# Kernel optimization log

Measured on AMD Instinct MI355X. Metric: run time of the kernel, lower is better.

## Reference

```python
import jax, jax.numpy as jnp
import numpy as np

B, R, L, K = 64, 196, 512, 768
NEG = jnp.float32(-2**31 + 1)


def setup_inputs() -> dict:
    key = jax.random.key(0)
    ks = jax.random.split(key, 8)
    image_emb = jax.random.normal(ks[0], (B, R, L), dtype=jnp.float32)
    seq_emb = jax.random.normal(ks[1], (B, L, K), dtype=jnp.float32)
    mask = jax.random.randint(ks[2], (B, L), 0, 2, dtype=jnp.int32)
    # Linear(l,1) and Linear(k,1) params, Xavier-ish scale
    image_W = jax.random.normal(ks[3], (L, 1), dtype=jnp.float32) / np.sqrt(L)
    image_b = jnp.zeros((1,), dtype=jnp.float32)
    seq_W = jax.random.normal(ks[4], (K, 1), dtype=jnp.float32) / np.sqrt(K)
    seq_b = jnp.zeros((1,), dtype=jnp.float32)
    # V_weight [L, L], xavier_uniform
    lim = np.sqrt(6.0 / (L + L)).astype(np.float32)
    V_weight = jax.random.uniform(ks[5], (L, L), dtype=jnp.float32, minval=-lim, maxval=lim)
    return {"image_emb": image_emb, "seq_emb": seq_emb, "mask": mask,
            "image_W": image_W, "image_b": image_b,
            "seq_W": seq_W, "seq_b": seq_b, "V_weight": V_weight}


def reference(image_emb, seq_emb, mask, image_W, image_b, seq_W, seq_b, V_weight):
    # p: [B,R,1], q: [B,L,1]
    p = jnp.tanh(image_emb @ image_W + image_b)
    q = jnp.tanh(seq_emb @ seq_W + seq_b)
    qt = jnp.swapaxes(q, 1, 2)              # [B,1,L]
    emb = p @ qt + qt                       # [B,R,L] (rank-1 outer + broadcast add)
    score = emb @ V_weight                  # [B,R,L]
    # dropout_rate=0.0 -> identity
    score = jnp.where(mask[:, None, :] == 0, NEG, score)
    score = jax.nn.softmax(score, axis=-1)  # [B,R,L]
    out = score @ seq_emb                   # [B,R,K]
    out = out / jnp.sqrt(jnp.float32(seq_emb.shape[-1]))
    return out
```

## Files before the change

### kernel.cpp

```cpp
#include <hip/hip_runtime.h>
#include <cstdint>
#include <cstddef>


typedef __attribute__((ext_vector_type(8))) short short8;
typedef __attribute__((ext_vector_type(4))) float f32x4;

__device__ __forceinline__ unsigned short f32_to_bf16(float x) {
    unsigned int u = __float_as_uint(x);
    unsigned int r = (u + 0x7FFFu + ((u >> 16) & 1u)) >> 16;
    return (unsigned short)r;
}
__device__ __forceinline__ float bf16_to_f32(unsigned short h) {
    return __uint_as_float(((unsigned int)h) << 16);
}

#if defined(__has_builtin)
#if __has_builtin(__builtin_amdgcn_cvt_pk_bf16_f32)
#define HAVE_PK_BF16 1
#endif
#endif

__device__ __forceinline__ unsigned int pk_bf16(float a, float b) {
#ifdef HAVE_PK_BF16
    typedef __attribute__((ext_vector_type(2))) __bf16 bf16x2;
    bf16x2 v = __builtin_amdgcn_cvt_pk_bf16_f32(a, b);
    return __builtin_bit_cast(unsigned int, v);
#else
    return (unsigned int)f32_to_bf16(a) | ((unsigned int)f32_to_bf16(b) << 16);
#endif
}

__global__ __launch_bounds__(256) void kprep(const float* __restrict__ seq,
                                             const float* __restrict__ seqW,
                                             const float* __restrict__ seqBias,
                                             const float* __restrict__ img,
                                             const float* __restrict__ imgW,
                                             const float* __restrict__ imgBias,
                                             unsigned short* __restrict__ seqT,
                                             float* __restrict__ qv,
                                             float* __restrict__ pv) {
    __shared__ __align__(16) unsigned int sT[128 * 32];
    __shared__ __align__(16) float sW[768];

    if (blockIdx.x >= 512) {
        int wv = threadIdx.x >> 6, lane = threadIdx.x & 63;
        int row = (blockIdx.x - 512) * 4 + wv;
        const float4* x4 = (const float4*)(img + (size_t)row * 512);
        const float4* w4 = (const float4*)imgW;
        float s = 0.f;
#pragma unroll
        for (int i = 0; i < 2; ++i) {
            float4 a = x4[i * 64 + lane];
            float4 c = w4[i * 64 + lane];
            s += a.x * c.x + a.y * c.y + a.z * c.z + a.w * c.w;
        }
#pragma unroll
        for (int o = 32; o; o >>= 1) s += __shfl_xor(s, o, 64);
        if (lane == 0) pv[row] = tanhf(s + imgBias[0]);
        return;
    }

    int b = blockIdx.x >> 3, jt = blockIdx.x & 7;
    int j0 = jt * 64;
    int t = threadIdx.x;
    sW[t] = seqW[t]; sW[t + 256] = seqW[t + 256]; sW[t + 512] = seqW[t + 512];

    int quad = t >> 4, kseg = t & 15;
    int qk = quad ^ kseg;
    const float* base = seq + (size_t)b * 512 * 768 + (size_t)(j0 + quad * 4) * 768;
    int jg = t & 7, krow = t >> 3;
    unsigned short* dst0 = seqT + (size_t)b * 768 * 512 + j0;
    float qp[4] = {0.f, 0.f, 0.f, 0.f};
    __syncthreads();

    for (int ck = 0; ck < 6; ++ck) {
        if (ck) __syncthreads();
#pragma unroll
        for (int rp = 0; rp < 2; ++rp) {
            int kq = rp * 64 + kseg * 4;
            int kg = ck * 128 + kq;
            float4 r0 = *(const float4*)(base + 0 * 768 + kg);
            float4 r1 = *(const float4*)(base + 1 * 768 + kg);
            float4 r2 = *(const float4*)(base + 2 * 768 + kg);
            float4 r3 = *(const float4*)(base + 3 * 768 + kg);
            float4 w  = *(const float4*)(sW + kg);
            qp[0] += r0.x * w.x + r0.y * w.y + r0.z * w.z + r0.w * w.w;
            qp[1] += r1.x * w.x + r1.y * w.y + r1.z * w.z + r1.w * w.w;
            qp[2] += r2.x * w.x + r2.y * w.y + r2.z * w.z + r2.w * w.w;
            qp[3] += r3.x * w.x + r3.y * w.y + r3.z * w.z + r3.w * w.w;
            float a0[4] = {r0.x, r0.y, r0.z, r0.w};
            float a1[4] = {r1.x, r1.y, r1.z, r1.w};
            float a2[4] = {r2.x, r2.y, r2.z, r2.w};
            float a3[4] = {r3.x, r3.y, r3.z, r3.w};
#pragma unroll
            for (int i = 0; i < 4; ++i) {
                int k = kq + i;
                int col = (qk ^ (i << 2)) & 15;
                uint2 v;
                v.x = pk_bf16(a0[i], a1[i]);
                v.y = pk_bf16(a2[i], a3[i]);
                *(uint2*)(sT + k * 32 + col * 2) = v;
            }
        }
        __syncthreads();
        unsigned short* dst = dst0 + (size_t)ck * 128 * 512;
#pragma unroll
        for (int wp = 0; wp < 4; ++wp) {
            int k = wp * 32 + krow;
            int s = ((k >> 2) & 15) ^ ((k & 3) << 2);
            int c0 = ((jg << 1) ^ s) & 15;
            int c1 = ((jg << 1) ^ 1 ^ s) & 15;
            uint2 va = *(const uint2*)(sT + k * 32 + c0 * 2);
            uint2 vb = *(const uint2*)(sT + k * 32 + c1 * 2);
            uint4 o;
            o.x = va.x; o.y = va.y; o.z = vb.x; o.w = vb.y;
            *(uint4*)(dst + (size_t)k * 512 + jg * 8) = o;
        }
    }
#pragma unroll
    for (int rr = 0; rr < 4; ++rr) {
        float s = qp[rr];
        s += __shfl_xor(s, 8, 64);
        s += __shfl_xor(s, 4, 64);
        s += __shfl_xor(s, 2, 64);
        s += __shfl_xor(s, 1, 64);
        if (kseg == 0) qv[b * 512 + j0 + quad * 4 + rr] = tanhf(s + seqBias[0]);
    }
}

__global__ __launch_bounds__(256) void krows_p(const float* __restrict__ x,
                                               const float* __restrict__ w,
                                               const float* __restrict__ bias,
                                               float* __restrict__ outp) {
    int wv = threadIdx.x >> 6, lane = threadIdx.x & 63;
    int row = blockIdx.x * 4 + wv;
    const float4* x4 = (const float4*)(x + (size_t)row * 512);
    const float4* w4 = (const float4*)w;
    float s = 0.f;
#pragma unroll
    for (int i = 0; i < 2; ++i) {
        float4 a = x4[i * 64 + lane];
        float4 c = w4[i * 64 + lane];
        s += a.x * c.x + a.y * c.y + a.z * c.z + a.w * c.w;
    }
#pragma unroll
    for (int o = 32; o; o >>= 1) s += __shfl_xor(s, o, 64);
    if (lane == 0) outp[row] = tanhf(s + bias[0]);
}

__global__ __launch_bounds__(256) void krows_q(const float* __restrict__ x,
                                               const float* __restrict__ w,
                                               const float* __restrict__ bias,
                                               float* __restrict__ outp) {
    int wv = threadIdx.x >> 6, lane = threadIdx.x & 63;
    int row = blockIdx.x * 4 + wv;
    const float4* x4 = (const float4*)(x + (size_t)row * 768);
    const float4* w4 = (const float4*)w;
    float s = 0.f;
#pragma unroll
    for (int i = 0; i < 3; ++i) {
        float4 a = x4[i * 64 + lane];
        float4 c = w4[i * 64 + lane];
        s += a.x * c.x + a.y * c.y + a.z * c.z + a.w * c.w;
    }
#pragma unroll
    for (int o = 32; o; o >>= 1) s += __shfl_xor(s, o, 64);
    if (lane == 0) outp[row] = tanhf(s + bias[0]);
}

__global__ __launch_bounds__(256) void kw(const float* __restrict__ qv,
                                          const float* __restrict__ V,
                                          const int* __restrict__ mask,
                                          float* __restrict__ wm) {
    __shared__ __align__(16) float sq[512];
    __shared__ __align__(16) float sacc[8][32][4];
    int b = blockIdx.x >> 2, jc = blockIdx.x & 3;
    int t = threadIdx.x;
    sq[t] = qv[b * 512 + t];
    sq[t + 256] = qv[b * 512 + t + 256];
    __syncthreads();
    int jt = t & 31, lg = t >> 5;
    const float4* V4 = (const float4*)V;
    int col4 = jc * 32 + jt;
    float ax = 0.f, ay = 0.f, az = 0.f, aw = 0.f;
    int lbase = lg * 64;
#pragma unroll 8
    for (int li = 0; li < 64; ++li) {
        int l = lbase + li;
        float qq = sq[l];
        float4 v = V4[(size_t)l * 128 + col4];
        ax += qq * v.x; ay += qq * v.y; az += qq * v.z; aw += qq * v.w;
    }
    sacc[lg][jt][0] = ax; sacc[lg][jt][1] = ay;
    sacc[lg][jt][2] = az; sacc[lg][jt][3] = aw;
    __syncthreads();
    if (t < 32) {
        float sx = 0.f, sy = 0.f, sz = 0.f, sw = 0.f;
#pragma unroll
        for (int g = 0; g < 8; ++g) {
            sx += sacc[g][t][0]; sy += sacc[g][t][1];
            sz += sacc[g][t][2]; sw += sacc[g][t][3];
        }
        const int* mrow = mask + b * 512 + jc * 128 + t * 4;
        float4 o;
        o.x = mrow[0] ? sx : -1e30f;
        o.y = mrow[1] ? sy : -1e30f;
        o.z = mrow[2] ? sz : -1e30f;
        o.w = mrow[3] ? sw : -1e30f;
        ((float4*)(wm + b * 512 + jc * 128))[t] = o;
    }
}

__global__ __launch_bounds__(256, 2) void kattn2(const unsigned short* __restrict__ seqT,
                                                 const float* __restrict__ p,
                                                 const float* __restrict__ wm,
                                                 float* __restrict__ out) {
    __shared__ __align__(16) unsigned short sB[2][128 * 64];
    __shared__ __align__(16) float swm[512];
    __shared__ float sinvz[64];
    __shared__ float sred[16];

    int raw = blockIdx.x;
    int g  = ((raw >> 5) << 3) + (raw & 7);
    int rt = (raw >> 3) & 3;
    int b  = g / 6, nt = g - b * 6;
    int t  = threadIdx.x;
    int wv = t >> 6, lane = t & 63;
    int mm = lane & 15, q = lane >> 4;
    int nb = nt * 128;

    float v0 = wm[b * 512 + t];
    float v1 = wm[b * 512 + t + 256];
    swm[t] = v0; swm[t + 256] = v1;
    float lmax = fmaxf(v0, v1);
    float fa = (v0 > -1e29f) ? v0 : 1e30f;
    float fb = (v1 > -1e29f) ? v1 : 1e30f;
    float lmin = fminf(fa, fb);
#pragma unroll
    for (int o = 32; o; o >>= 1) {
        lmax = fmaxf(lmax, __shfl_xor(lmax, o, 64));
        lmin = fminf(lmin, __shfl_xor(lmin, o, 64));
    }
    if (lane == 0) { sred[wv] = lmax; sred[8 + wv] = lmin; }
    __syncthreads();
    float wmax = fmaxf(fmaxf(sred[0], sred[1]), fmaxf(sred[2], sred[3]));
    float wmin = fminf(fminf(sred[8], sred[9]), fminf(sred[10], sred[11]));

    int rl = wv * 16 + mm;
    int r  = rt * 64 + rl;
    bool valid = r < 196;
    int pidx = b * 196 + (valid ? r : 195);
    float c = 1.0f + p[pidx];
    float M = (c >= 0.f) ? c * wmax : c * wmin;

    short8 afrag[16];
    float zsum = 0.f;
    const f32x4* swm4 = (const f32x4*)swm;
#pragma unroll
    for (int tk = 0; tk < 16; ++tk) {
        int jb = tk * 32 + q * 8;
        f32x4 w0 = swm4[jb >> 2];
        f32x4 w1 = swm4[(jb >> 2) + 1];
        short8 af;
#pragma unroll
        for (int jj = 0; jj < 8; ++jj) {
            float ww = (jj < 4) ? w0[jj] : w1[jj - 4];
            float e = valid ? __expf(c * ww - M) : 0.f;
            unsigned short h = f32_to_bf16(e);
            zsum += bf16_to_f32(h);
            af[jj] = (short)h;
        }
        afrag[tk] = af;
    }
    zsum += __shfl_xor(zsum, 16, 64);
    zsum += __shfl_xor(zsum, 32, 64);
    if (q == 0) sinvz[rl] = 1.0f / zsum;

    f32x4 acc[8];
#pragma unroll
    for (int s = 0; s < 8; ++s) acc[s] = (f32x4){0.f, 0.f, 0.f, 0.f};

    const unsigned short* seqTb = seqT + (size_t)b * 768 * 512 + (size_t)nb * 512;
    int nrow = t >> 3, jg = t & 7;
    auto stage = [&](int ch, int buf) {
        unsigned short* sb = sB[buf];
#pragma unroll
        for (int pp = 0; pp < 4; ++pp) {
            int n = pp * 32 + nrow;
            short8 v = *(const short8*)(seqTb + (size_t)n * 512 + ch * 64 + jg * 8);
            int sw = (n ^ (n >> 3)) & 7;
            *(short8*)(sb + n * 64 + ((jg ^ sw) << 3)) = v;
        }
    };

    __syncthreads();
    stage(0, 0);
    __syncthreads();
#pragma unroll
    for (int ch = 0; ch < 8; ++ch) {
        if (ch < 7) stage(ch + 1, (ch + 1) & 1);
        const unsigned short* cb = sB[ch & 1];
#pragma unroll
        for (int kk = 0; kk < 2; ++kk) {
            short8 bfr[8];
#pragma unroll
            for (int s = 0; s < 8; ++s) {
                int n = s * 16 + mm;
                int sw = (n ^ (n >> 3)) & 7;
                bfr[s] = *(const short8*)(cb + n * 64 + ((((kk << 2) + q) ^ sw) << 3));
            }
#pragma unroll
            for (int s = 0; s < 8; ++s)
                acc[s] = __builtin_amdgcn_mfma_f32_16x16x32_bf16(
                    afrag[(ch << 1) + kk], bfr[s], acc[s], 0, 0, 0);
        }
        __syncthreads();
    }

    const float invsqrtk = 0.036084391824351615f;
#pragma unroll
    for (int reg = 0; reg < 4; ++reg) {
        int row = q * 4 + reg;
        int rr = rt * 64 + wv * 16 + row;
        if (rr < 196) {
            float scale = sinvz[wv * 16 + row] * invsqrtk;
            float* op = out + (size_t)(b * 196 + rr) * 768 + nb + mm;
#pragma unroll
            for (int s = 0; s < 8; ++s)
                op[s * 16] = acc[s][reg] * scale;
        }
    }
}

__global__ __launch_bounds__(256, 2) void kattn(const float* __restrict__ seq,
                                                const float* __restrict__ p,
                                                const float* __restrict__ wm,
                                                float* __restrict__ out) {
    __shared__ __align__(16) unsigned int sseq[2][128 * 32];
    __shared__ __align__(16) float swm[512];
    __shared__ float sinvz[64];
    __shared__ float sred[16];

    int id = blockIdx.x;
    int rt = id & 3;
    int nt = (id >> 2) % 6;
    int b  = id / 24;
    int t  = threadIdx.x;
    int wv = t >> 6, lane = t & 63;
    int mm = lane & 15, q = lane >> 4;
    int nb = nt * 128;

    float v0 = wm[b * 512 + t];
    float v1 = wm[b * 512 + t + 256];
    swm[t] = v0; swm[t + 256] = v1;
    float lmax = fmaxf(v0, v1);
    float fa = (v0 > -1e29f) ? v0 : 1e30f;
    float fb = (v1 > -1e29f) ? v1 : 1e30f;
    float lmin = fminf(fa, fb);
#pragma unroll
    for (int o = 32; o; o >>= 1) {
        lmax = fmaxf(lmax, __shfl_xor(lmax, o, 64));
        lmin = fminf(lmin, __shfl_xor(lmin, o, 64));
    }
    if (lane == 0) { sred[wv] = lmax; sred[8 + wv] = lmin; }
    __syncthreads();
    float wmax = fmaxf(fmaxf(sred[0], sred[1]), fmaxf(sred[2], sred[3]));
    float wmin = fminf(fminf(sred[8], sred[9]), fminf(sred[10], sred[11]));

    int rl = wv * 16 + mm;
    int r  = rt * 64 + rl;
    bool valid = r < 196;
    int pidx = b * 196 + (valid ? r : 195);
    float c = 1.0f + p[pidx];
    float M = (c >= 0.f) ? c * wmax : c * wmin;

    short8 afrag[16];
    float zsum = 0.f;
    const f32x4* swm4 = (const f32x4*)swm;
#pragma unroll
    for (int tk = 0; tk < 16; ++tk) {
        int jb = tk * 32 + q * 8;
        f32x4 w0 = swm4[jb >> 2];
        f32x4 w1 = swm4[(jb >> 2) + 1];
        short8 af;
#pragma unroll
        for (int jj = 0; jj < 8; ++jj) {
            float ww = (jj < 4) ? w0[jj] : w1[jj - 4];
            float e = valid ? __expf(c * ww - M) : 0.f;
            unsigned short h = f32_to_bf16(e);
            zsum += bf16_to_f32(h);
            af[jj] = (short)h;
        }
        afrag[tk] = af;
    }
    zsum += __shfl_xor(zsum, 16, 64);
    zsum += __shfl_xor(zsum, 32, 64);
    if (q == 0) sinvz[rl] = 1.0f / zsum;

    f32x4 acc[8];
#pragma unroll
    for (int s = 0; s < 8; ++s) acc[s] = (f32x4){0.f, 0.f, 0.f, 0.f};

    const float* seqb = seq + (size_t)b * 512 * 768 + nb;
    int tl = t & 31, jp = t >> 5;
    int n0 = tl * 4;
    auto stage = [&](int ch, int buf) {
        unsigned int* sb = sseq[buf];
#pragma unroll
        for (int pass = 0; pass < 4; ++pass) {
            int jl = pass * 16 + jp * 2;
            int jglob = ch * 64 + jl;
            float4 a0 = *(const float4*)(seqb + (size_t)jglob * 768 + n0);
            float4 a1 = *(const float4*)(seqb + (size_t)(jglob + 1) * 768 + n0);
            float a0v[4] = {a0.x, a0.y, a0.z, a0.w};
            float a1v[4] = {a1.x, a1.y, a1.z, a1.w};
            int g = jl >> 3;
            int wo = (jl & 7) >> 1;
#pragma unroll
            for (int i = 0; i < 4; ++i) {
                int n = n0 + i;
                int sw = (n ^ (n >> 3)) & 7;
                unsigned int pk = (unsigned int)f32_to_bf16(a0v[i]) |
                                  ((unsigned int)f32_to_bf16(a1v[i]) << 16);
                sb[n * 32 + ((g ^ sw) << 2) + wo] = pk;
            }
        }
    };

    __syncthreads();
    stage(0, 0);
    __syncthreads();
#pragma unroll
    for (int ch = 0; ch < 8; ++ch) {
        if (ch < 7) stage(ch + 1, (ch + 1) & 1);
        const unsigned int* cb = sseq[ch & 1];
#pragma unroll
        for (int kk = 0; kk < 2; ++kk) {
            short8 bfr[8];
#pragma unroll
            for (int s = 0; s < 8; ++s) {
                int n = s * 16 + mm;
                int g = kk * 4 + q;
                int sw = (n ^ (n >> 3)) & 7;
                bfr[s] = *(const short8*)(cb + n * 32 + ((g ^ sw) << 2));
            }
#pragma unroll
            for (int s = 0; s < 8; ++s)
                acc[s] = __builtin_amdgcn_mfma_f32_16x16x32_bf16(
                    afrag[ch * 2 + kk], bfr[s], acc[s], 0, 0, 0);
        }
        __syncthreads();
    }

    const float invsqrtk = 0.036084391824351615f;
#pragma unroll
    for (int reg = 0; reg < 4; ++reg) {
        int row = q * 4 + reg;
        int rr = rt * 64 + wv * 16 + row;
        if (rr < 196) {
            float scale = sinvz[wv * 16 + row] * invsqrtk;
            float* op = out + (size_t)(b * 196 + rr) * 768 + nb + mm;
#pragma unroll
            for (int s = 0; s < 8; ++s)
                op[s * 16] = acc[s][reg] * scale;
        }
    }
}

extern "C" void kernel_launch(void* const* d_in, const int* in_sizes, int n_in,
                              void* d_out, int out_size, void* d_ws, size_t ws_size,
                              hipStream_t stream) {
    const float* image_emb = (const float*)d_in[0];
    const float* seq_emb   = (const float*)d_in[1];
    const int*   mask      = (const int*)d_in[2];
    const float* image_W   = (const float*)d_in[3];
    const float* image_b   = (const float*)d_in[4];
    const float* seq_W     = (const float*)d_in[5];
    const float* seq_b     = (const float*)d_in[6];
    const float* V         = (const float*)d_in[7];
    float* out = (float*)d_out;

    float* p_ws  = (float*)d_ws;
    float* q_ws  = (float*)((char*)d_ws + (64 << 10));
    float* wm_ws = (float*)((char*)d_ws + (192 << 10));
    unsigned short* seqT = (unsigned short*)((char*)d_ws + (384 << 10));

    size_t need = (size_t)(384 << 10) + (size_t)64 * 768 * 512 * 2;
    if (ws_size >= need) {
        kprep<<<dim3(3648), dim3(256), 0, stream>>>(seq_emb, seq_W, seq_b,
                                                    image_emb, image_W, image_b,
                                                    seqT, q_ws, p_ws);
        kw<<<dim3(256), dim3(256), 0, stream>>>(q_ws, V, mask, wm_ws);
        kattn2<<<dim3(1536), dim3(256), 0, stream>>>(seqT, p_ws, wm_ws, out);
    } else {
        krows_p<<<dim3(3136), dim3(256), 0, stream>>>(image_emb, image_W, image_b, p_ws);
        krows_q<<<dim3(8192), dim3(256), 0, stream>>>(seq_emb, seq_W, seq_b, q_ws);
        kw<<<dim3(256), dim3(256), 0, stream>>>(q_ws, V, mask, wm_ws);
        kattn<<<dim3(1536), dim3(256), 0, stream>>>(seq_emb, p_ws, wm_ws, out);
    }
}
```

Measured before the change: 239.1 us.

## Split seq transpose/projection across K chunks with atomic partial sums

```diff
diff --git a/kernel.cpp b/kernel.cpp
--- a/kernel.cpp
+++ b/kernel.cpp
@@ -33,19 +33,18 @@
 
 __global__ __launch_bounds__(256) void kprep(const float* __restrict__ seq,
                                              const float* __restrict__ seqW,
-                                             const float* __restrict__ seqBias,
                                              const float* __restrict__ img,
                                              const float* __restrict__ imgW,
                                              const float* __restrict__ imgBias,
                                              unsigned short* __restrict__ seqT,
-                                             float* __restrict__ qv,
+                                             float* __restrict__ qacc,
                                              float* __restrict__ pv) {
     __shared__ __align__(16) unsigned int sT[128 * 32];
-    __shared__ __align__(16) float sW[768];
-
-    if (blockIdx.x >= 512) {
+    __shared__ __align__(16) float sWc[128];
+
+    if (blockIdx.x >= 3072) {
         int wv = threadIdx.x >> 6, lane = threadIdx.x & 63;
-        int row = (blockIdx.x - 512) * 4 + wv;
+        int row = (blockIdx.x - 3072) * 4 + wv;
         const float4* x4 = (const float4*)(img + (size_t)row * 512);
         const float4* w4 = (const float4*)imgW;
         float s = 0.f;
@@ -61,62 +60,59 @@
         return;
     }
 
-    int b = blockIdx.x >> 3, jt = blockIdx.x & 7;
+    int id = blockIdx.x;
+    int b = id / 48, rem = id - b * 48;
+    int jt = rem / 6, ck = rem - jt * 6;
     int j0 = jt * 64;
     int t = threadIdx.x;
-    sW[t] = seqW[t]; sW[t + 256] = seqW[t + 256]; sW[t + 512] = seqW[t + 512];
+    if (t < 128) sWc[t] = seqW[ck * 128 + t];
 
     int quad = t >> 4, kseg = t & 15;
     int qk = quad ^ kseg;
-    const float* base = seq + (size_t)b * 512 * 768 + (size_t)(j0 + quad * 4) * 768;
+    const float* base = seq + (size_t)b * 512 * 768 + (size_t)(j0 + quad * 4) * 768 + ck * 128;
     int jg = t & 7, krow = t >> 3;
-    unsigned short* dst0 = seqT + (size_t)b * 768 * 512 + j0;
     float qp[4] = {0.f, 0.f, 0.f, 0.f};
     __syncthreads();
 
-    for (int ck = 0; ck < 6; ++ck) {
-        if (ck) __syncthreads();
-#pragma unroll
-        for (int rp = 0; rp < 2; ++rp) {
-            int kq = rp * 64 + kseg * 4;
-            int kg = ck * 128 + kq;
-            float4 r0 = *(const float4*)(base + 0 * 768 + kg);
-            float4 r1 = *(const float4*)(base + 1 * 768 + kg);
-            float4 r2 = *(const float4*)(base + 2 * 768 + kg);
-            float4 r3 = *(const float4*)(base + 3 * 768 + kg);
-            float4 w  = *(const float4*)(sW + kg);
-            qp[0] += r0.x * w.x + r0.y * w.y + r0.z * w.z + r0.w * w.w;
-            qp[1] += r1.x * w.x + r1.y * w.y + r1.z * w.z + r1.w * w.w;
-            qp[2] += r2.x * w.x + r2.y * w.y + r2.z * w.z + r2.w * w.w;
-            qp[3] += r3.x * w.x + r3.y * w.y + r3.z * w.z + r3.w * w.w;
-            float a0[4] = {r0.x, r0.y, r0.z, r0.w};
-            float a1[4] = {r1.x, r1.y, r1.z, r1.w};
-            float a2[4] = {r2.x, r2.y, r2.z, r2.w};
-            float a3[4] = {r3.x, r3.y, r3.z, r3.w};
-#pragma unroll
-            for (int i = 0; i < 4; ++i) {
-                int k = kq + i;
-                int col = (qk ^ (i << 2)) & 15;
-                uint2 v;
-                v.x = pk_bf16(a0[i], a1[i]);
-                v.y = pk_bf16(a2[i], a3[i]);
-                *(uint2*)(sT + k * 32 + col * 2) = v;
-            }
-        }
-        __syncthreads();
-        unsigned short* dst = dst0 + (size_t)ck * 128 * 512;
-#pragma unroll
-        for (int wp = 0; wp < 4; ++wp) {
-            int k = wp * 32 + krow;
-            int s = ((k >> 2) & 15) ^ ((k & 3) << 2);
-            int c0 = ((jg << 1) ^ s) & 15;
-            int c1 = ((jg << 1) ^ 1 ^ s) & 15;
-            uint2 va = *(const uint2*)(sT + k * 32 + c0 * 2);
-            uint2 vb = *(const uint2*)(sT + k * 32 + c1 * 2);
-            uint4 o;
-            o.x = va.x; o.y = va.y; o.z = vb.x; o.w = vb.y;
-            *(uint4*)(dst + (size_t)k * 512 + jg * 8) = o;
-        }
+#pragma unroll
+    for (int rp = 0; rp < 2; ++rp) {
+        int kq = rp * 64 + kseg * 4;
+        float4 r0 = *(const float4*)(base + 0 * 768 + kq);
+        float4 r1 = *(const float4*)(base + 1 * 768 + kq);
+        float4 r2 = *(const float4*)(base + 2 * 768 + kq);
+        float4 r3 = *(const float4*)(base + 3 * 768 + kq);
+        float4 w  = *(const float4*)(sWc + kq);
+        qp[0] += r0.x * w.x + r0.y * w.y + r0.z * w.z + r0.w * w.w;
+        qp[1] += r1.x * w.x + r1.y * w.y + r1.z * w.z + r1.w * w.w;
+        qp[2] += r2.x * w.x + r2.y * w.y + r2.z * w.z + r2.w * w.w;
+        qp[3] += r3.x * w.x + r3.y * w.y + r3.z * w.z + r3.w * w.w;
+        float a0[4] = {r0.x, r0.y, r0.z, r0.w};
+        float a1[4] = {r1.x, r1.y, r1.z, r1.w};
+        float a2[4] = {r2.x, r2.y, r2.z, r2.w};
+        float a3[4] = {r3.x, r3.y, r3.z, r3.w};
+#pragma unroll
+        for (int i = 0; i < 4; ++i) {
+            int k = kq + i;
+            int col = (qk ^ (i << 2)) & 15;
+            uint2 v;
+            v.x = pk_bf16(a0[i], a1[i]);
+            v.y = pk_bf16(a2[i], a3[i]);
+            *(uint2*)(sT + k * 32 + col * 2) = v;
+        }
+    }
+    __syncthreads();
+    unsigned short* dst = seqT + (size_t)b * 768 * 512 + (size_t)ck * 128 * 512 + j0;
+#pragma unroll
+    for (int wp = 0; wp < 4; ++wp) {
+        int k = wp * 32 + krow;
+        int s = ((k >> 2) & 15) ^ ((k & 3) << 2);
+        int c0 = ((jg << 1) ^ s) & 15;
+        int c1 = ((jg << 1) ^ 1 ^ s) & 15;
+        uint2 va = *(const uint2*)(sT + k * 32 + c0 * 2);
+        uint2 vb = *(const uint2*)(sT + k * 32 + c1 * 2);
+        uint4 o;
+        o.x = va.x; o.y = va.y; o.z = vb.x; o.w = vb.y;
+        *(uint4*)(dst + (size_t)k * 512 + jg * 8) = o;
     }
 #pragma unroll
     for (int rr = 0; rr < 4; ++rr) {
@@ -125,7 +121,7 @@
         s += __shfl_xor(s, 4, 64);
         s += __shfl_xor(s, 2, 64);
         s += __shfl_xor(s, 1, 64);
-        if (kseg == 0) qv[b * 512 + j0 + quad * 4 + rr] = tanhf(s + seqBias[0]);
+        if (kseg == 0) atomicAdd(qacc + b * 512 + j0 + quad * 4 + rr, s);
     }
 }
 
@@ -151,7 +147,6 @@
 
 __global__ __launch_bounds__(256) void krows_q(const float* __restrict__ x,
                                                const float* __restrict__ w,
-                                               const float* __restrict__ bias,
                                                float* __restrict__ outp) {
     int wv = threadIdx.x >> 6, lane = threadIdx.x & 63;
     int row = blockIdx.x * 4 + wv;
@@ -166,10 +161,11 @@
     }
 #pragma unroll
     for (int o = 32; o; o >>= 1) s += __shfl_xor(s, o, 64);
-    if (lane == 0) outp[row] = tanhf(s + bias[0]);
-}
-
-__global__ __launch_bounds__(256) void kw(const float* __restrict__ qv,
+    if (lane == 0) outp[row] = s;
+}
+
+__global__ __launch_bounds__(256) void kw(const float* __restrict__ qacc,
+                                          const float* __restrict__ seqBias,
                                           const float* __restrict__ V,
                                           const int* __restrict__ mask,
                                           float* __restrict__ wm) {
@@ -177,8 +173,9 @@
     __shared__ __align__(16) float sacc[8][32][4];
     int b = blockIdx.x >> 2, jc = blockIdx.x & 3;
     int t = threadIdx.x;
-    sq[t] = qv[b * 512 + t];
-    sq[t + 256] = qv[b * 512 + t + 256];
+    float qb = seqBias[0];
+    sq[t] = tanhf(qacc[b * 512 + t] + qb);
+    sq[t + 256] = tanhf(qacc[b * 512 + t + 256] + qb);
     __syncthreads();
     int jt = t & 31, lg = t >> 5;
     const float4* V4 = (const float4*)V;
@@ -488,15 +485,16 @@
 
     size_t need = (size_t)(384 << 10) + (size_t)64 * 768 * 512 * 2;
     if (ws_size >= need) {
-        kprep<<<dim3(3648), dim3(256), 0, stream>>>(seq_emb, seq_W, seq_b,
+        hipMemsetAsync(q_ws, 0, 512 * 64 * sizeof(float), stream);
+        kprep<<<dim3(6208), dim3(256), 0, stream>>>(seq_emb, seq_W,
                                                     image_emb, image_W, image_b,
                                                     seqT, q_ws, p_ws);
-        kw<<<dim3(256), dim3(256), 0, stream>>>(q_ws, V, mask, wm_ws);
+        kw<<<dim3(256), dim3(256), 0, stream>>>(q_ws, seq_b, V, mask, wm_ws);
         kattn2<<<dim3(1536), dim3(256), 0, stream>>>(seqT, p_ws, wm_ws, out);
     } else {
         krows_p<<<dim3(3136), dim3(256), 0, stream>>>(image_emb, image_W, image_b, p_ws);
-        krows_q<<<dim3(8192), dim3(256), 0, stream>>>(seq_emb, seq_W, seq_b, q_ws);
-        kw<<<dim3(256), dim3(256), 0, stream>>>(q_ws, V, mask, wm_ws);
+        krows_q<<<dim3(8192), dim3(256), 0, stream>>>(seq_emb, seq_W, q_ws);
+        kw<<<dim3(256), dim3(256), 0, stream>>>(q_ws, seq_b, V, mask, wm_ws);
         kattn<<<dim3(1536), dim3(256), 0, stream>>>(seq_emb, p_ws, wm_ws, out);
     }
 }
```

Result: faster. 233.4 us (-2.4%).
